# Kernel tuning notes

Hardware: AMD Instinct MI355X
Metric: run time of the kernel (lower is better)

Reference implementation:

```python
import jax, jax.numpy as jnp
import numpy as np

B, N, T, NUM_API = 4, 160, 512, 20000  # queries, list length, tag vocab size, number of APIs
TAG_DENSITY = 0.05


def _compute_lambda(y_score, tag_set, M):
    # y_score: [N]; tag_set: [N,T] multi-hot rows api_tag_embedding[y_pred]; M: [T] multi-hot target.
    # Faithful to mode == 'cover' branch of LambdaRankLoss.compute_lambda.
    n = tag_set.shape[0]
    f32 = tag_set.dtype
    idx = jnp.arange(n)
    log_values = jnp.log2(jnp.arange(2, n + 2, dtype=f32))             # [N]
    P = jax.lax.cummax(tag_set, axis=0)                                # set_union_list = cummax(tag_set) [N,T]
    Mc = (jnp.count_nonzero(M) + 1).astype(f32)                        # M_nonzero_count
    # count_nonzero(clamp(M - set_union_list[k], min=0)) == #(M_t > P[k,t])
    cU = jnp.sum(M[None, :] > P, axis=1).astype(f32)                   # [N]

    # pre[i] = rowwise-max of tag_set[:i-1]. Torch quirk: i==0 -> tag_set[:-1] (all but last row); i==1 -> empty.
    pre = jnp.where(idx[:, None] == 0, P[n - 2][None, :],
                    jnp.where(idx[:, None] == 1, jnp.zeros((), f32),
                              P[jnp.clip(idx - 2, 0, n - 1)]))         # [N,T] (0 is max-identity: entries >= 0)

    # R[a,b] = max(tag_set[a..b]) along rows; 0 when b < a (rows before a masked to 0, then cummax)
    masked = jnp.where(idx[None, :, None] >= idx[:, None, None], tag_set[None, :, :], jnp.zeros((), f32))
    R = jax.lax.cummax(masked, axis=1)                                 # [N,N,T]

    # mid[k,i] = max(tag_set[i+1:k]) = R[i+1, k-1] when k >= i+2, else empty -> 0
    i_ix = idx[None, :]
    k_ix = idx[:, None]
    mid = jnp.where((k_ix >= i_ix + 2)[:, :, None],
                    R[jnp.clip(i_ix + 1, 0, n - 1), jnp.clip(k_ix - 1, 0, n - 1)],
                    jnp.zeros((), f32))                                # [K,I,T]

    # A[k,i] = max(cat(tag_set[:i-1], tag_set[i+1:k]));  Q[k,i,j] = max(A[k,i], tag_set[j])
    A = jnp.maximum(pre[None, :, :], mid)                              # [K,I,T]
    # count_nonzero(clamp(M - Q[k,i,j], 0)) = sum_t [M_t > A[k,i,t]] * [M_t > tag_set[j,t]]
    aM = (M[None, None, :] > A).astype(f32)                            # [K,I,T]
    bM = (M[None, :] > tag_set).astype(f32)                            # [J,T]
    cQ = jnp.einsum('kit,jt->kij', aM, bM)                             # [K,I,J] Q_nonzero counts

    W = (cU[:, None, None] - cQ) / (Mc * log_values[:, None, None])    # [K,I,J]
    # Z1[i,j] = sum_{k=i}^{j-1} W[k,i,j]  (strictly upper-triangular in (i,j))
    maskZ = (idx[None, :, None] <= idx[:, None, None]) & (idx[:, None, None] < idx[None, None, :])
    Z1 = jnp.sum(jnp.where(maskZ, W, jnp.zeros((), f32)), axis=0)      # [I,J]

    # lambda1[i,j] = 1 / (1 + exp(s_i - s_j))
    lam = 1.0 / (1.0 + jnp.exp(y_score[:, None] - y_score[None, :]))
    return jnp.sum(lam * Z1) / jnp.asarray(n + 1, f32)


def setup_inputs() -> dict:
    key = jax.random.key(0)
    k1, k2, k3, k4 = jax.random.split(key, 4)
    y_scores = jax.random.normal(k1, (B, N), jnp.float32)
    y_preds = jax.random.randint(k2, (B, N), 0, NUM_API)
    M = (jax.random.uniform(k3, (B, T)) < TAG_DENSITY).astype(jnp.float32)
    api_tag_embedding = (jax.random.uniform(k4, (NUM_API, T)) < TAG_DENSITY).astype(jnp.float32)
    return {"y_scores": y_scores, "M": M, "api_tag_embedding": api_tag_embedding, "y_preds": y_preds}


def reference(y_scores, M, api_tag_embedding, y_preds):
    def per_query(s, m, pred):
        return _compute_lambda(s, api_tag_embedding[pred], m)
    vals = jax.vmap(per_query)(y_scores, M, y_preds)  # [B]
    return jnp.mean(vals)  # loss / len(y_scores)
```

## Files before the change

### kernel.cpp

```cpp
#include <hip/hip_runtime.h>
#include <stdint.h>

typedef unsigned long long u64;

constexpr int B_ = 4;
constexpr int N_ = 160;
constexpr int T_ = 512;
constexpr int W_ = T_ / 64;

__global__ __launch_bounds__(64) void pack_all(const float* __restrict__ emb,
                                               const int* __restrict__ preds,
                                               const float* __restrict__ Mf,
                                               u64* __restrict__ tags,
                                               u64* __restrict__ Mp,
                                               double* __restrict__ accD,
                                               int* __restrict__ cnt) {
    int row  = blockIdx.x;
    int lane = threadIdx.x;
    if (row < B_ * N_) {
        const float* src = emb + (long long)preds[row] * T_;
#pragma unroll
        for (int w = 0; w < W_; ++w) {
            u64 m = __ballot(src[w * 64 + lane] != 0.0f);
            if (lane == 0) tags[(long long)row * W_ + w] = m;
        }
    } else {
        int b = row - B_ * N_;
        const float* src = Mf + (long long)b * T_;
#pragma unroll
        for (int w = 0; w < W_; ++w) {
            u64 m = __ballot(src[w * 64 + lane] != 0.0f);
            if (lane == 0) Mp[b * W_ + w] = m;
        }
        if (b == 0 && lane == 0) { accD[0] = 0.0; cnt[0] = 0; }
    }
}

__global__ __launch_bounds__(256) void lambda_main(const u64* __restrict__ tags,
                                                   const u64* __restrict__ Mp,
                                                   const float* __restrict__ scores,
                                                   double* __restrict__ accD,
                                                   int* __restrict__ cnt,
                                                   float* __restrict__ out) {
    constexpr int LD = N_ + 1;
    __shared__ u64 Tsh[W_ * LD];
    __shared__ u64 U[W_ * LD];
    __shared__ u64 V[W_ * LD];
    __shared__ u64 bT[W_ * LD];
    __shared__ u64 Msh[W_];
    __shared__ float scoresL[N_];
    __shared__ float redF[4];
    __shared__ float cUsh, Mcsh;

    const int k   = blockIdx.x;
    const int b   = blockIdx.y;
    const int tid = threadIdx.x;

    if (tid < W_)  Msh[tid]     = Mp[b * W_ + tid];
    if (tid < N_)  scoresL[tid] = scores[b * N_ + tid];

    for (int x = tid; x < W_ * N_; x += 256) {
        int r = x >> 3, w = x & 7;
        Tsh[w * LD + r] = tags[(long long)b * N_ * W_ + x];
    }
    __syncthreads();

    for (int x = tid; x < W_ * N_; x += 256) {
        int r = x >> 3, w = x & 7;
        bT[w * LD + r] = Msh[w] & ~Tsh[w * LD + r];
    }

    u64* rd = Tsh;
    u64* wr = U;
    for (int d = 1; d < k; d <<= 1) {
        for (int x = tid; x < W_ * k; x += 256) {
            int r = x >> 3, w = x & 7;
            u64 v = rd[w * LD + r];
            if (r + d < k) v |= rd[w * LD + r + d];
            wr[w * LD + r] = v;
        }
        __syncthreads();
        rd = wr;
        wr = (rd == U) ? V : U;
    }
    u64* suf = rd;
    u64* freebuf = wr;

    u64* prd = Tsh;
    u64* pwr = freebuf;
    for (int d = 1; d < N_; d <<= 1) {
        for (int x = tid; x < W_ * N_; x += 256) {
            int r = x >> 3, w = x & 7;
            u64 v = prd[w * LD + r];
            if (r >= d) v |= prd[w * LD + r - d];
            pwr[w * LD + r] = v;
        }
        __syncthreads();
        u64* t = prd; prd = pwr; pwr = t;
    }

    u64* aw = pwr;
    for (int x = tid; x < W_ * (k + 1); x += 256) {
        int i = x >> 3, w = x & 7;
        u64 pre;
        if (i == 1) pre = 0ull;
        else {
            int sr = (i == 0) ? (N_ - 2) : (i - 2);
            pre = prd[w * LD + sr];
        }
        u64 sv = (i + 1 < k) ? suf[w * LD + i + 1] : 0ull;
        aw[w * LD + i] = Msh[w] & ~pre & ~sv;
    }
    if (tid == 0) {
        int c = 0, cm = 0;
#pragma unroll
        for (int w = 0; w < W_; ++w) {
            c  += __popcll(Msh[w] & ~prd[w * LD + k]);
            cm += __popcll(Msh[w]);
        }
        cUsh = (float)c;
        Mcsh = (float)(cm + 1);
    }
    __syncthreads();

    const int m = N_ - 1 - k;
    float accLam = 0.0f, accC = 0.0f;
    if (m > 0) {
        const int npairs = (k + 1) * m;
        if (tid < npairs) {
            int cntp = (npairs - tid + 255) >> 8;
            int i   = tid / m;
            int jj  = tid - i * m;
            const int di = 256 / m;
            const int rj = 256 - di * m;
            for (int c = 0; c < cntp; ++c) {
                const int j = k + 1 + jj;
                int cc = 0;
#pragma unroll
                for (int w = 0; w < W_; ++w)
                    cc += __popcll(aw[w * LD + i] & bT[w * LD + j]);
                float lam = 1.0f / (1.0f + __expf(scoresL[i] - scoresL[j]));
                accLam += lam;
                accC   += lam * (float)cc;
                i += di; jj += rj;
                if (jj >= m) { jj -= m; ++i; }
            }
        }
    }

    float val = cUsh * accLam - accC;
    for (int off = 32; off >= 1; off >>= 1) val += __shfl_down(val, off, 64);
    if ((tid & 63) == 0) redF[tid >> 6] = val;
    __syncthreads();
    if (tid == 0) {
        float s = redF[0] + redF[1] + redF[2] + redF[3];
        float invlog = 1.0f / log2f((float)(k + 2));
        double v = (double)(s * invlog) / (double)Mcsh;
        atomicAdd(accD, v);
        __threadfence();
        int c = atomicAdd(cnt, 1);
        if (c == B_ * N_ - 1) {
            double total = atomicAdd(accD, 0.0);
            out[0] = (float)(total / ((double)(N_ + 1) * (double)B_));
        }
    }
}

extern "C" void kernel_launch(void* const* d_in, const int* in_sizes, int n_in,
                              void* d_out, int out_size, void* d_ws, size_t ws_size,
                              hipStream_t stream) {
    const float* y_scores = (const float*)d_in[0];
    const float* Mf       = (const float*)d_in[1];
    const float* emb      = (const float*)d_in[2];
    const int*   preds    = (const int*)d_in[3];
    float* out = (float*)d_out;

    u64* tags   = (u64*)d_ws;
    u64* Mp     = tags + (size_t)B_ * N_ * W_;
    double* accD = (double*)(Mp + B_ * W_);
    int* cnt    = (int*)(accD + 1);

    pack_all<<<B_ * N_ + B_, 64, 0, stream>>>(emb, preds, Mf, tags, Mp, accD, cnt);
    dim3 grid(N_, B_);
    lambda_main<<<grid, 256, 0, stream>>>(tags, Mp, y_scores, accD, cnt, out);
}
```

Baseline: 111.3 us.

## Fuse prefix/suffix scans, shorten prefix to k+1 rows, contiguous pair chunks

The prefix-OR scan now covers only rows 0..k instead of all N rows, and it runs in the same barrier-separated steps as the suffix scan, with the first doubling step folded into the bT pass. The special row-0 term (prefix up to N-2) is rebuilt from the k-limited prefix plus a reduced tail OR. The pair loop gives each thread a contiguous chunk of (i,j) pairs so the A row and score_i stay in registers and are reloaded only when i changes. This cuts scan work and the number of __syncthreads per block, at the cost of an extra shared buffer and more complex indexing.

```diff
diff --git a/kernel.cpp b/kernel.cpp
--- a/kernel.cpp
+++ b/kernel.cpp
@@ -46,8 +46,10 @@
     __shared__ u64 Tsh[W_ * LD];
     __shared__ u64 U[W_ * LD];
     __shared__ u64 V[W_ * LD];
+    __shared__ u64 AW[W_ * LD];
     __shared__ u64 bT[W_ * LD];
     __shared__ u64 Msh[W_];
+    __shared__ u64 tailT[32];
     __shared__ float scoresL[N_];
     __shared__ float redF[4];
     __shared__ float cUsh, Mcsh;
@@ -67,59 +69,76 @@
 
     for (int x = tid; x < W_ * N_; x += 256) {
         int r = x >> 3, w = x & 7;
-        bT[w * LD + r] = Msh[w] & ~Tsh[w * LD + r];
-    }
-
-    u64* rd = Tsh;
-    u64* wr = U;
-    for (int d = 1; d < k; d <<= 1) {
+        u64 t = Tsh[w * LD + r];
+        bT[w * LD + r] = Msh[w] & ~t;
+        if (r <= k) {
+            u64 v = t;
+            if (r >= 1) v |= Tsh[w * LD + r - 1];
+            U[w * LD + r] = v;
+        }
+        if (r < k) {
+            u64 v = t;
+            if (r + 1 < k) v |= Tsh[w * LD + r + 1];
+            V[w * LD + r] = v;
+        }
+    }
+    __syncthreads();
+
+    u64* ps = U;  u64* pd = Tsh;
+    u64* ss = V;  u64* sd = AW;
+    for (int d = 2; d < k + 1; d <<= 1) {
+        for (int x = tid; x < W_ * (k + 1); x += 256) {
+            int r = x >> 3, w = x & 7;
+            u64 v = ps[w * LD + r];
+            if (r >= d) v |= ps[w * LD + r - d];
+            pd[w * LD + r] = v;
+        }
         for (int x = tid; x < W_ * k; x += 256) {
             int r = x >> 3, w = x & 7;
-            u64 v = rd[w * LD + r];
-            if (r + d < k) v |= rd[w * LD + r + d];
-            wr[w * LD + r] = v;
+            u64 v = ss[w * LD + r];
+            if (r + d < k) v |= ss[w * LD + r + d];
+            sd[w * LD + r] = v;
         }
         __syncthreads();
-        rd = wr;
-        wr = (rd == U) ? V : U;
-    }
-    u64* suf = rd;
-    u64* freebuf = wr;
-
-    u64* prd = Tsh;
-    u64* pwr = freebuf;
-    for (int d = 1; d < N_; d <<= 1) {
-        for (int x = tid; x < W_ * N_; x += 256) {
-            int r = x >> 3, w = x & 7;
-            u64 v = prd[w * LD + r];
-            if (r >= d) v |= prd[w * LD + r - d];
-            pwr[w * LD + r] = v;
-        }
-        __syncthreads();
-        u64* t = prd; prd = pwr; pwr = t;
-    }
-
-    u64* aw = pwr;
+        u64* t1 = ps; ps = pd; pd = t1;
+        u64* t2 = ss; ss = sd; sd = t2;
+    }
+
+    {
+        int w = tid & 7, g = tid >> 3;
+        u64 acc = 0;
+        for (int r = k + 1 + g; r <= N_ - 2; r += 32) acc |= Tsh[w * LD + r];
+        acc |= __shfl_down(acc, 8, 64);
+        acc |= __shfl_down(acc, 16, 64);
+        acc |= __shfl_down(acc, 32, 64);
+        if ((tid & 63) < 8) tailT[(tid >> 6) * 8 + w] = acc;
+    }
     for (int x = tid; x < W_ * (k + 1); x += 256) {
         int i = x >> 3, w = x & 7;
-        u64 pre;
-        if (i == 1) pre = 0ull;
-        else {
-            int sr = (i == 0) ? (N_ - 2) : (i - 2);
-            pre = prd[w * LD + sr];
-        }
-        u64 sv = (i + 1 < k) ? suf[w * LD + i + 1] : 0ull;
-        aw[w * LD + i] = Msh[w] & ~pre & ~sv;
+        if (i >= 1) {
+            u64 pre = (i == 1) ? 0ull : ps[w * LD + i - 2];
+            u64 sv  = (i + 1 < k) ? ss[w * LD + i + 1] : 0ull;
+            pd[w * LD + i] = Msh[w] & ~pre & ~sv;
+        }
     }
     if (tid == 0) {
         int c = 0, cm = 0;
 #pragma unroll
         for (int w = 0; w < W_; ++w) {
-            c  += __popcll(Msh[w] & ~prd[w * LD + k]);
+            c  += __popcll(Msh[w] & ~ps[w * LD + k]);
             cm += __popcll(Msh[w]);
         }
         cUsh = (float)c;
         Mcsh = (float)(cm + 1);
+    }
+    __syncthreads();
+    if (tid < 8) {
+        int w = tid;
+        u64 pn2 = (k >= N_ - 2)
+                    ? ps[w * LD + (N_ - 2)]
+                    : (ps[w * LD + k] | tailT[w] | tailT[8 + w] | tailT[16 + w] | tailT[24 + w]);
+        u64 sv0 = (1 < k) ? ss[w * LD + 1] : 0ull;
+        pd[w * LD + 0] = Msh[w] & ~pn2 & ~sv0;
     }
     __syncthreads();
 
@@ -127,23 +146,33 @@
     float accLam = 0.0f, accC = 0.0f;
     if (m > 0) {
         const int npairs = (k + 1) * m;
-        if (tid < npairs) {
-            int cntp = (npairs - tid + 255) >> 8;
-            int i   = tid / m;
-            int jj  = tid - i * m;
-            const int di = 256 / m;
-            const int rj = 256 - di * m;
-            for (int c = 0; c < cntp; ++c) {
+        const int chunk  = (npairs + 255) >> 8;
+        int q0 = tid * chunk;
+        int q1 = q0 + chunk; if (q1 > npairs) q1 = npairs;
+        if (q0 < q1) {
+            int i  = q0 / m;
+            int jj = q0 - i * m;
+            u64 a[8];
+#pragma unroll
+            for (int w = 0; w < 8; ++w) a[w] = pd[w * LD + i];
+            float si = scoresL[i];
+            for (int q = q0; q < q1; ++q) {
                 const int j = k + 1 + jj;
                 int cc = 0;
 #pragma unroll
-                for (int w = 0; w < W_; ++w)
-                    cc += __popcll(aw[w * LD + i] & bT[w * LD + j]);
-                float lam = 1.0f / (1.0f + __expf(scoresL[i] - scoresL[j]));
+                for (int w = 0; w < 8; ++w)
+                    cc += __popcll(a[w] & bT[w * LD + j]);
+                float lam = 1.0f / (1.0f + __expf(si - scoresL[j]));
                 accLam += lam;
                 accC   += lam * (float)cc;
-                i += di; jj += rj;
-                if (jj >= m) { jj -= m; ++i; }
+                if (++jj == m) {
+                    jj = 0; ++i;
+                    if (q + 1 < q1) {
+#pragma unroll
+                        for (int w = 0; w < 8; ++w) a[w] = pd[w * LD + i];
+                        si = scoresL[i];
+                    }
+                }
             }
         }
     }
@@ -175,10 +204,10 @@
     const int*   preds    = (const int*)d_in[3];
     float* out = (float*)d_out;
 
-    u64* tags   = (u64*)d_ws;
-    u64* Mp     = tags + (size_t)B_ * N_ * W_;
+    u64* tags    = (u64*)d_ws;
+    u64* Mp      = tags + (size_t)B_ * N_ * W_;
     double* accD = (double*)(Mp + B_ * W_);
-    int* cnt    = (int*)(accD + 1);
+    int* cnt     = (int*)(accD + 1);
 
     pack_all<<<B_ * N_ + B_, 64, 0, stream>>>(emb, preds, Mf, tags, Mp, accD, cnt);
     dim3 grid(N_, B_);
```

After: 113.3 us. Within noise of the previous version (+1.8%).
